# Optimization experiments

Measured on AMD Instinct MI355X. Metric: run time of the kernel, lower is better.

## Reference

```python
import jax, jax.numpy as jnp
import numpy as np

VOCAB, EMB, HDIM, VDIM, ATT = 30000, 256, 512, 128, 256
B, N, T = 64, 196, 32


def setup_inputs() -> dict:
    key = jax.random.key(0)
    ks = jax.random.split(key, 8)
    s = 0.02
    return {
        "V": jax.random.normal(ks[0], (B, N, VDIM), jnp.float32),
        "y": jax.random.randint(ks[1], (B, T), 0, VOCAB),
        "embed": jax.random.normal(ks[2], (VOCAB, EMB), jnp.float32) * s,
        "att_W_w": jax.random.normal(ks[3], (ATT, HDIM), jnp.float32) * s,
        "att_W_b": jnp.zeros((ATT,), jnp.float32),
        "att_U_w": jax.random.normal(ks[4], (ATT, VDIM), jnp.float32) * s,
        "att_U_b": jnp.zeros((ATT,), jnp.float32),
        "att_v_w": jax.random.normal(ks[5], (1, ATT), jnp.float32) * s,
        "att_v_b": jnp.zeros((1,), jnp.float32),
        "W_ih": jax.random.normal(ks[6], (4 * HDIM, EMB + VDIM), jnp.float32) * s,
        "W_hh": jax.random.normal(ks[7], (4 * HDIM, HDIM), jnp.float32) * s,
        "b_ih": jnp.zeros((4 * HDIM,), jnp.float32),
        "b_hh": jnp.zeros((4 * HDIM,), jnp.float32),
        "proj_w": jax.random.normal(jax.random.fold_in(key, 9), (EMB, HDIM), jnp.float32) * s,
    }


def reference(V, y, embed, att_W_w, att_W_b, att_U_w, att_U_b, att_v_w, att_v_b,
              W_ih, W_hh, b_ih, b_hh, proj_w):
    Bsz = y.shape[0]
    hdim = W_hh.shape[1]
    # loop-invariant U(V): [B, N, ATT]
    UV = jnp.einsum('bnv,av->bna', V, att_U_w) + att_U_b

    def step(carry, y_t):
        h, c, x_t = carry
        # additive attention
        Wh = h @ att_W_w.T + att_W_b                      # [B, ATT]
        e = jnp.tanh(Wh[:, None, :] + UV) @ att_v_w.T + att_v_b  # [B, N, 1]
        a = jax.nn.softmax(e, axis=1)
        ctx = jnp.sum(a * V, axis=1)                      # [B, VDIM]
        # LSTMCell (PyTorch gate order i, f, g, o)
        xc = jnp.concatenate([x_t, ctx], axis=-1)
        gates = xc @ W_ih.T + b_ih + h @ W_hh.T + b_hh
        i, f, g, o = jnp.split(gates, 4, axis=-1)
        c_new = jax.nn.sigmoid(f) * c + jax.nn.sigmoid(i) * jnp.tanh(g)
        h_new = jax.nn.sigmoid(o) * jnp.tanh(c_new)
        # dropout is identity in eval mode
        e_t = h_new @ proj_w.T                            # [B, EMB]
        logit = e_t @ embed.T                             # [B, VOCAB]
        x_next = embed[y_t]                               # teacher forcing
        return (h_new, c_new, x_next), logit

    h0 = jnp.zeros((Bsz, hdim), V.dtype)
    c0 = jnp.zeros((Bsz, hdim), V.dtype)
    x0 = embed[y[:, 0]]
    _, logits = jax.lax.scan(step, (h0, c0, x0), y[:, 1:].T)  # [T-1, B, VOCAB]
    return jnp.transpose(logits, (1, 0, 2))
```

## Files before the change

### kernel.cpp

```cpp
#include <hip/hip_runtime.h>
#include <stdint.h>

typedef unsigned short u16;
typedef uint32_t u32;
typedef short s16x8 __attribute__((ext_vector_type(8)));
typedef float f32x4 __attribute__((ext_vector_type(4)));

#define DEV __device__ __forceinline__

#define TSCALE 2.885390082f

DEV float bf2f(u16 h){ union{u32 u; float f;} x; x.u = ((u32)h)<<16; return x.f; }
DEV u16 f2bf(float f){ union{float f; u32 u;} x; x.f = f; u32 u = x.u;
  return (u16)((u + 0x7fffu + ((u>>16)&1u))>>16); }
DEV float bflo(u32 w){ union{u32 u; float f;} x; x.u = w<<16; return x.f; }
DEV float bfhi(u32 w){ union{u32 u; float f;} x; x.u = w & 0xffff0000u; return x.f; }

DEV float exp2_fast(float x){ return __builtin_amdgcn_exp2f(x); }
DEV float rcp_fast(float x){ return __builtin_amdgcn_rcpf(x); }
DEV float tanh2(float x){ float t = exp2_fast(TSCALE*x);
  return fmaf(-2.f, rcp_fast(t + 1.f), 1.f); }
DEV float sig2(float x){ return rcp_fast(1.f + exp2_fast(-1.442695041f*x)); }

DEV u32   ld_u(const u32* p){ return __hip_atomic_load(p, __ATOMIC_RELAXED, __HIP_MEMORY_SCOPE_AGENT); }
DEV void  st_u(u32* p, u32 v){ __hip_atomic_store(p, v, __ATOMIC_RELAXED, __HIP_MEMORY_SCOPE_AGENT); }

__global__ void f2b_kernel(const float* __restrict__ src, u16* __restrict__ dst, int n4, float scale){
  int i = blockIdx.x*blockDim.x + threadIdx.x;
  if (i < n4) {
    float4 v = ((const float4*)src)[i];
    ushort4 o; o.x = f2bf(v.x*scale); o.y = f2bf(v.y*scale); o.z = f2bf(v.z*scale); o.w = f2bf(v.w*scale);
    ((ushort4*)dst)[i] = o;
  }
}

__global__ void prep_wih2b(const float* __restrict__ Wih, u16* __restrict__ Wc){
  int idx = blockIdx.x*256 + threadIdx.x;
  int j = idx>>7, k = idx&127;
  Wc[idx] = f2bf(Wih[(size_t)j*384 + 256 + k]);
}

__global__ void repack_h(const u16* __restrict__ H2, u16* __restrict__ Hl){
  int r = blockIdx.x;
  int s = r>>6, b = r&63;
  int tid = threadIdx.x;
  u32 v = *((const u32*)(H2 + (size_t)(s+1)*32768 + (size_t)(tid>>2)*512 + (size_t)b*8) + (tid&3));
  ((u32*)(Hl + (size_t)r*512))[tid] = v;
}

__global__ __launch_bounds__(256) void gemm_bt(
    const u16* __restrict__ A, int lda,
    const u16* __restrict__ B, int ldb,
    const float* __restrict__ bias1, const float* __restrict__ bias2, float bscale,
    void* __restrict__ C, int ldc,
    int M, int N, int K, int Mt, int mode)
{
  __shared__ __align__(16) u16 As[64*64];
  __shared__ __align__(16) u16 Bs[128*64];
  int nwg = (int)gridDim.x;
  int b0 = blockIdx.x;
  int qq = nwg >> 3, rr = nwg & 7;
  int bswz;
  if (qq == 0) bswz = b0;
  else {
    int xcd = b0 & 7, i = b0 >> 3;
    bswz = (xcd < rr) ? (xcd*(qq+1) + i) : (rr*(qq+1) + (xcd - rr)*qq + i);
  }
  int mt = bswz % Mt, nt = bswz / Mt;
  int m0 = mt*64, n0 = nt*128;
  int tid = threadIdx.x, wave = tid>>6, lane = tid&63;
  int lrow = lane>>3, lcol = (lane&7)*8;
  f32x4 acc[2][4];
  #pragma unroll
  for (int i=0;i<2;i++)
    #pragma unroll
    for (int j=0;j<4;j++) acc[i][j] = (f32x4){0,0,0,0};
  int wm = (wave>>1)*32, wn = (wave&1)*64;
  int fr = lane&15, fk = (lane>>4)*8;
  for (int k0 = 0; k0 < K; k0 += 64) {
    __syncthreads();
    #pragma unroll
    for (int i = 0; i < 2; i++) {
      int ci = wave + i*4;
      int row = ci*8 + lrow;
      const u16* g = A + (size_t)(m0+row)*lda + k0 + lcol;
      __builtin_amdgcn_global_load_lds(
        (const __attribute__((address_space(1))) u32*)g,
        (__attribute__((address_space(3))) u32*)&As[ci*512], 16, 0, 0);
    }
    #pragma unroll
    for (int i = 0; i < 4; i++) {
      int ci = wave + i*4;
      int row = ci*8 + lrow;
      int gr = n0 + row; gr = gr < N ? gr : N-1;
      const u16* g = B + (size_t)gr*ldb + k0 + lcol;
      __builtin_amdgcn_global_load_lds(
        (const __attribute__((address_space(1))) u32*)g,
        (__attribute__((address_space(3))) u32*)&Bs[ci*512], 16, 0, 0);
    }
    __syncthreads();
    #pragma unroll
    for (int kk = 0; kk < 2; kk++) {
      s16x8 af[2], bfv[4];
      #pragma unroll
      for (int mi=0; mi<2; mi++)
        af[mi] = *(const s16x8*)&As[(wm + mi*16 + fr)*64 + kk*32 + fk];
      #pragma unroll
      for (int ni=0; ni<4; ni++)
        bfv[ni] = *(const s16x8*)&Bs[(wn + ni*16 + fr)*64 + kk*32 + fk];
      #pragma unroll
      for (int mi=0; mi<2; mi++)
        #pragma unroll
        for (int ni=0; ni<4; ni++)
          acc[mi][ni] = __builtin_amdgcn_mfma_f32_16x16x32_bf16(af[mi], bfv[ni], acc[mi][ni], 0,0,0);
    }
  }
  #pragma unroll
  for (int mi=0; mi<2; mi++)
    #pragma unroll
    for (int ni=0; ni<4; ni++) {
      int col = n0 + wn + ni*16 + (lane&15);
      if (col >= N) continue;
      float bv = 0.0f;
      if (bias1) bv += bias1[col];
      if (bias2) bv += bias2[col];
      bv *= bscale;
      int rbase = m0 + wm + mi*16 + ((lane>>4)<<2);
      #pragma unroll
      for (int r=0; r<4; r++) {
        int row = rbase + r;
        float v = acc[mi][ni][r] + bv;
        if (mode == 0) ((float*)C)[(size_t)row*ldc + col] = v;
        else if (mode == 1) ((u16*)C)[(size_t)row*ldc + col] = f2bf(v);
        else { int orow = (row&63)*31 + (row>>6); ((float*)C)[(size_t)orow*ldc + col] = v; }
      }
    }
}

__global__ void gather_x(const int* __restrict__ y, const float* __restrict__ embed, u16* __restrict__ X)
{
  int r = blockIdx.x;
  int s = r>>6, b = r&63;
  int tok = y[b*32 + s];
  X[(size_t)r*256 + threadIdx.x] = f2bf(embed[(size_t)tok*256 + threadIdx.x]);
}

#define NB 64

DEV void gbar(u32* flags, int bid, unsigned g){
  __asm__ volatile("" ::: "memory");
  __builtin_amdgcn_s_waitcnt(0);
  __syncthreads();
  if (threadIdx.x == 0) st_u(&flags[bid*16], g);
  if (threadIdx.x < 64) {
    for (;;) {
      u32 a = ld_u(&flags[threadIdx.x*16]);
      if (__all(a >= g)) break;
      __builtin_amdgcn_s_sleep(1);
    }
  }
  __syncthreads();
  __asm__ volatile("" ::: "memory");
}

__global__ __launch_bounds__(256, 1) void decoder_steps(
    const float* __restrict__ V,
    const float* __restrict__ attWb,
    const float* __restrict__ attvw,
    const float* __restrict__ attvb,
    const u16* __restrict__ WhhB,
    const u16* __restrict__ attWwB,
    const u16* __restrict__ WcB,
    u16* __restrict__ H2,
    const u16* __restrict__ UV,
    const u16* __restrict__ Xg,
    u16* __restrict__ CtxB,
    u32* __restrict__ flags)
{
  int bid = blockIdx.x, tid = threadIdx.x;
  int wave = tid>>6, lane = tid&63;
  int fr = lane&15, fkq = lane>>4;

  __shared__ __align__(16) u16 Wlds[32][648];
  __shared__ __align__(16) u16 Xglds[64][32];
  __shared__ float hls[512];
  __shared__ float whs[256];
  __shared__ float vws[256];
  __shared__ float esc[200];
  __shared__ float red1;
  __shared__ float part[256];

  {
    int r = tid>>3, p = tid&7;
    int grow = ((r>>3)<<9) + bid*8 + (r&7);
    #pragma unroll
    for (int i=0;i<10;i++){
      int k = p*80 + i*8;
      const u16* src = (k < 512) ? (WhhB + (size_t)grow*512 + k)
                                 : (WcB  + (size_t)grow*128 + (k-512));
      *(s16x8*)&Wlds[r][k] = *(const s16x8*)src;
    }
  }
  vws[tid] = attvw[tid];
  float vb = attvb[0];
  float c_reg[4] = {0.f,0.f,0.f,0.f};
  unsigned gen = 0;
  __syncthreads();

  int br = wave*16 + fr;

  for (int t = 0; t < 31; t++) {
    u32 hv = *((const u32*)(H2 + (size_t)t*32768 + (size_t)(tid>>2)*512 + (size_t)bid*8) + (tid&3));
    const u16* Hbase = H2 + (size_t)t*32768 + (size_t)br*8;
    s16x8 af[16];
    #pragma unroll
    for (int kt=0;kt<16;kt++) af[kt] = *(const s16x8*)(Hbase + (size_t)(kt*4+fkq)*512);
    s16x8 xg = *(const s16x8*)(Xg + (size_t)t*131072 + (size_t)(tid>>2)*2048 + (size_t)(tid&3)*512 + (size_t)bid*8);

    hls[2*tid]   = bflo(hv);
    hls[2*tid+1] = bfhi(hv);
    __syncthreads();

    {
      const u32* wr = (const u32*)(attWwB + (size_t)tid*512);
      float acc = TSCALE * attWb[tid];
      #pragma unroll 4
      for (int k=0;k<512;k+=8){
        u32 w0 = wr[(k>>1)+0], w1 = wr[(k>>1)+1], w2 = wr[(k>>1)+2], w3 = wr[(k>>1)+3];
        float4 h0 = *(const float4*)&hls[k];
        float4 h1 = *(const float4*)&hls[k+4];
        acc = fmaf(bflo(w0), h0.x, acc); acc = fmaf(bfhi(w0), h0.y, acc);
        acc = fmaf(bflo(w1), h0.z, acc); acc = fmaf(bfhi(w1), h0.w, acc);
        acc = fmaf(bflo(w2), h1.x, acc); acc = fmaf(bfhi(w2), h1.y, acc);
        acc = fmaf(bflo(w3), h1.z, acc); acc = fmaf(bfhi(w3), h1.w, acc);
      }
      whs[tid] = acc;
    }

    f32x4 a0 = (f32x4){0,0,0,0}, a1 = (f32x4){0,0,0,0};
    #pragma unroll
    for (int kt=0;kt<16;kt++){
      s16x8 b0 = *(const s16x8*)&Wlds[fr][kt*32 + fkq*8];
      s16x8 b1 = *(const s16x8*)&Wlds[16+fr][kt*32 + fkq*8];
      a0 = __builtin_amdgcn_mfma_f32_16x16x32_bf16(af[kt], b0, a0, 0,0,0);
      a1 = __builtin_amdgcn_mfma_f32_16x16x32_bf16(af[kt], b1, a1, 0,0,0);
    }
    __builtin_amdgcn_sched_barrier(0);
    __syncthreads();

    if (tid < 196) {
      const u32* uvp = (const u32*)(UV + ((size_t)bid*196 + tid)*256);
      float e = 0.0f;
      #pragma unroll 4
      for (int a = 0; a < 256; a += 4) {
        u32 uw0 = uvp[(a>>1)], uw1 = uvp[(a>>1)+1];
        float4 w4 = *(const float4*)&whs[a];
        float4 v4 = *(const float4*)&vws[a];
        float t0 = exp2_fast(w4.x + bflo(uw0));
        float t1 = exp2_fast(w4.y + bfhi(uw0));
        float t2 = exp2_fast(w4.z + bflo(uw1));
        float t3 = exp2_fast(w4.w + bfhi(uw1));
        e = fmaf(v4.x, fmaf(-2.f, rcp_fast(t0+1.f), 1.f), e);
        e = fmaf(v4.y, fmaf(-2.f, rcp_fast(t1+1.f), 1.f), e);
        e = fmaf(v4.z, fmaf(-2.f, rcp_fast(t2+1.f), 1.f), e);
        e = fmaf(v4.w, fmaf(-2.f, rcp_fast(t3+1.f), 1.f), e);
      }
      esc[tid] = exp2_fast(1.442695041f*(e + vb));
    }
    *(s16x8*)&Xglds[tid>>2][(tid&3)*8] = xg;
    __syncthreads();

    if (tid < 64) {
      float s = esc[tid] + esc[64+tid] + esc[128+tid];
      if (tid < 4)  s += esc[192+tid];
      #pragma unroll
      for (int off=32; off>=1; off>>=1) s += __shfl_xor(s, off);
      if (tid==0) red1 = s;
    }
    {
      int k = tid&127, hf = tid>>7;
      const float* vp = V + ((size_t)bid*196 + hf*98)*128 + k;
      float a = 0.f;
      for (int n2=0; n2<98; n2++) a = fmaf(esc[hf*98+n2], vp[(size_t)n2*128], a);
      part[tid] = a;
    }
    __syncthreads();

    if (tid < 64) {
      float inv = rcp_fast(red1);
      float c0 = (part[2*tid]   + part[128+2*tid]) * inv;
      float c1 = (part[2*tid+1] + part[129+2*tid]) * inv;
      u32 pk = (u32)f2bf(c0) | ((u32)f2bf(c1) << 16);
      st_u((u32*)(CtxB + (size_t)t*8192 + (size_t)bid*128) + tid, pk);
    }
    gen++; gbar(flags, bid, gen);

    {
      const u16* Crow = CtxB + (size_t)t*8192 + (size_t)br*128 + fkq*8;
      #pragma unroll
      for (int kt=0;kt<4;kt++){
        s16x8 cf = *(const s16x8*)(Crow + kt*32);
        s16x8 b0 = *(const s16x8*)&Wlds[fr][(16+kt)*32 + fkq*8];
        s16x8 b1 = *(const s16x8*)&Wlds[16+fr][(16+kt)*32 + fkq*8];
        a0 = __builtin_amdgcn_mfma_f32_16x16x32_bf16(cf, b0, a0, 0,0,0);
        a1 = __builtin_amdgcn_mfma_f32_16x16x32_bf16(cf, b1, a1, 0,0,0);
      }
      int c = fr;
      int xr0 = ((c>>3)&1)*8 + (c&7);
      float v0[4], v1[4], s0[4], s1[4];
      #pragma unroll
      for (int r=0;r<4;r++){
        int b_r = wave*16 + fkq*4 + r;
        v0[r] = a0[r] + bf2f(Xglds[b_r][xr0]);
        v1[r] = a1[r] + bf2f(Xglds[b_r][16+xr0]);
      }
      #pragma unroll
      for (int r=0;r<4;r++){ s0[r] = __shfl_xor(v0[r], 8); s1[r] = __shfl_xor(v1[r], 8); }
      if (c < 8) {
        #pragma unroll
        for (int r=0;r<4;r++){
          int b_r = wave*16 + fkq*4 + r;
          float ig = sig2(v0[r]);
          float fg = sig2(s0[r]);
          float gg = tanh2(v1[r]);
          float og = sig2(s1[r]);
          float cn = fmaf(fg, c_reg[r], ig*gg);
          c_reg[r] = cn;
          float hvv = og * tanh2(cn);
          float hp = __shfl_xor(hvv, 1);
          if (!(c&1)) {
            u32 pk = (u32)f2bf(hvv) | ((u32)f2bf(hp) << 16);
            st_u((u32*)(H2 + (size_t)(t+1)*32768 + (size_t)bid*512 + (size_t)b_r*8) + (c>>1), pk);
          }
        }
      }
    }
    if (t < 30) { gen++; gbar(flags, bid, gen); }
  }
}

#define OFF_H    1024u
#define OFF_UV   2098176u
#define OFF_X    8520704u
#define OFF_XG   9536512u
#define OFF_GH   17662976u
#define OFF_EMB  OFF_GH
#define OFF_WH   33915904u
#define OFF_E    35947520u
#define OFF_VB   36963328u
#define OFF_WIH  40174592u
#define OFF_WHH  41747456u
#define OFF_AWW  43844608u
#define OFF_AUW  44106752u
#define OFF_PRJ  44172288u

extern "C" void kernel_launch(void* const* d_in, const int* in_sizes, int n_in,
                              void* d_out, int out_size, void* d_ws, size_t ws_size,
                              hipStream_t stream)
{
  const float* V      = (const float*)d_in[0];
  const int*   y      = (const int*)  d_in[1];
  const float* embed  = (const float*)d_in[2];
  const float* attWw  = (const float*)d_in[3];
  const float* attWb  = (const float*)d_in[4];
  const float* attUw  = (const float*)d_in[5];
  const float* attUb  = (const float*)d_in[6];
  const float* attvw  = (const float*)d_in[7];
  const float* attvb  = (const float*)d_in[8];
  const float* Wih    = (const float*)d_in[9];
  const float* Whh    = (const float*)d_in[10];
  const float* bih    = (const float*)d_in[11];
  const float* bhh    = (const float*)d_in[12];
  const float* projw  = (const float*)d_in[13];
  float* out = (float*)d_out;
  char* ws = (char*)d_ws;

  u16*   H2   = (u16*)  (ws + OFF_H);
  u16*   UVb  = (u16*)  (ws + OFF_UV);
  u16*   Xb   = (u16*)  (ws + OFF_X);
  u16*   Xg   = (u16*)  (ws + OFF_XG);
  u16*   Hl   = (u16*)  (ws + OFF_XG);
  u32*   flags= (u32*)  (ws + OFF_WH);
  u16*   CtxB = (u16*)  (ws + OFF_WH + 8192);
  u16*   E    = (u16*)  (ws + OFF_E);
  u16*   Vb   = (u16*)  (ws + OFF_VB);
  u16*   WcB  = (u16*)  (ws + OFF_VB);
  u16*   embB = (u16*)  (ws + OFF_EMB);
  u16*   WihB = (u16*)  (ws + OFF_WIH);
  u16*   WhhB = (u16*)  (ws + OFF_WHH);
  u16*   attWwB = (u16*)(ws + OFF_AWW);
  u16*   attUwB = (u16*)(ws + OFF_AUW);
  u16*   projB  = (u16*)(ws + OFF_PRJ);

  hipMemsetAsync(ws + OFF_H, 0, 65536, stream);
  hipMemsetAsync(ws + OFF_WH, 0, 4096, stream);

  f2b_kernel<<<(401408+255)/256, 256, 0, stream>>>(V,     Vb,     401408, 1.0f);
  f2b_kernel<<<(196608+255)/256, 256, 0, stream>>>(Wih,   WihB,   196608, 1.0f);
  f2b_kernel<<<(262144+255)/256, 256, 0, stream>>>(Whh,   WhhB,   262144, 1.0f);
  f2b_kernel<<<(32768+255)/256,  256, 0, stream>>>(attWw, attWwB,  32768, TSCALE);
  f2b_kernel<<<(8192+255)/256,   256, 0, stream>>>(attUw, attUwB,   8192, TSCALE);
  f2b_kernel<<<(32768+255)/256,  256, 0, stream>>>(projw, projB,   32768, 1.0f);

  gather_x<<<1984, 256, 0, stream>>>(y, embed, Xb);

  gemm_bt<<<196*2, 256, 0, stream>>>(Vb, 128, attUwB, 128, attUb, nullptr, TSCALE,
                                     UVb, 256, 12544, 256, 128, 196, 1);
  prep_wih2b<<<1024, 256, 0, stream>>>(Wih, WcB);
  gemm_bt<<<31*16, 256, 0, stream>>>(Xb, 256, WihB, 384, bih, bhh, 1.0f,
                                     Xg, 2048, 1984, 2048, 256, 31, 1);

  decoder_steps<<<NB, 256, 0, stream>>>(V, attWb, attvw, attvb,
      WhhB, attWwB, WcB, H2, UVb, Xg, CtxB, flags);

  f2b_kernel<<<(1920000+255)/256, 256, 0, stream>>>(embed, embB, 1920000, 1.0f);

  repack_h<<<1984, 256, 0, stream>>>(H2, Hl);

  gemm_bt<<<31*2, 256, 0, stream>>>(Hl, 512, projB, 512, nullptr, nullptr, 1.0f,
                                    E, 256, 1984, 256, 512, 31, 1);
  gemm_bt<<<31*235, 256, 0, stream>>>(E, 256, embB, 256, nullptr, nullptr, 1.0f,
                                      out, 30000, 1984, 30000, 256, 31, 2);
}
```

Before: 1.015 ms.

## Double decoder block width to 512 threads and split attention reductions

The persistent decoder kernel now runs 512 threads per block instead of 256. The extra waves take over the H/Xg staging loads while the first four waves load MFMA fragments. The W·h matvec and the attention energy loop are each split in half across thread pairs and combined with a shuffle, and the context reduction is split four ways over the N dimension. This is meant to shorten the serial per-step latency on the 64-block critical path, at the cost of more threads idling during the MFMA phases and extra barrier participants. The embedding bf16 conversion is also moved to run before the decoder instead of after it, which only reorders independent work.

```diff
diff --git a/kernel.cpp b/kernel.cpp
--- a/kernel.cpp
+++ b/kernel.cpp
@@ -163,7 +163,7 @@
   __asm__ volatile("" ::: "memory");
 }
 
-__global__ __launch_bounds__(256, 1) void decoder_steps(
+__global__ __launch_bounds__(512, 1) void decoder_steps(
     const float* __restrict__ V,
     const float* __restrict__ attWb,
     const float* __restrict__ attvw,
@@ -188,20 +188,20 @@
   __shared__ float vws[256];
   __shared__ float esc[200];
   __shared__ float red1;
-  __shared__ float part[256];
+  __shared__ float part[512];
 
   {
-    int r = tid>>3, p = tid&7;
+    int r = tid>>4, p = tid&15;
     int grow = ((r>>3)<<9) + bid*8 + (r&7);
     #pragma unroll
-    for (int i=0;i<10;i++){
-      int k = p*80 + i*8;
+    for (int i=0;i<5;i++){
+      int k = p*40 + i*8;
       const u16* src = (k < 512) ? (WhhB + (size_t)grow*512 + k)
                                  : (WcB  + (size_t)grow*128 + (k-512));
       *(s16x8*)&Wlds[r][k] = *(const s16x8*)src;
     }
   }
-  vws[tid] = attvw[tid];
+  if (tid < 256) vws[tid] = attvw[tid];
   float vb = attvb[0];
   float c_reg[4] = {0.f,0.f,0.f,0.f};
   unsigned gen = 0;
@@ -210,64 +210,78 @@
   int br = wave*16 + fr;
 
   for (int t = 0; t < 31; t++) {
-    u32 hv = *((const u32*)(H2 + (size_t)t*32768 + (size_t)(tid>>2)*512 + (size_t)bid*8) + (tid&3));
-    const u16* Hbase = H2 + (size_t)t*32768 + (size_t)br*8;
     s16x8 af[16];
-    #pragma unroll
-    for (int kt=0;kt<16;kt++) af[kt] = *(const s16x8*)(Hbase + (size_t)(kt*4+fkq)*512);
-    s16x8 xg = *(const s16x8*)(Xg + (size_t)t*131072 + (size_t)(tid>>2)*2048 + (size_t)(tid&3)*512 + (size_t)bid*8);
-
-    hls[2*tid]   = bflo(hv);
-    hls[2*tid+1] = bfhi(hv);
+    s16x8 xg;
+    if (tid < 256) {
+      const u16* Hbase = H2 + (size_t)t*32768 + (size_t)br*8;
+      #pragma unroll
+      for (int kt=0;kt<16;kt++) af[kt] = *(const s16x8*)(Hbase + (size_t)(kt*4+fkq)*512);
+    } else {
+      int t2 = tid - 256;
+      u32 hv = *((const u32*)(H2 + (size_t)t*32768 + (size_t)(t2>>2)*512 + (size_t)bid*8) + (t2&3));
+      hls[2*t2]   = bflo(hv);
+      hls[2*t2+1] = bfhi(hv);
+      xg = *(const s16x8*)(Xg + (size_t)t*131072 + (size_t)(t2>>2)*2048 + (size_t)(t2&3)*512 + (size_t)bid*8);
+    }
     __syncthreads();
 
     {
-      const u32* wr = (const u32*)(attWwB + (size_t)tid*512);
-      float acc = TSCALE * attWb[tid];
+      int a_ = tid>>1, kh = (tid&1)*256;
+      const u32* wr = (const u32*)(attWwB + (size_t)a_*512 + kh);
+      float acc = (tid&1) ? 0.f : TSCALE * attWb[a_];
       #pragma unroll 4
-      for (int k=0;k<512;k+=8){
+      for (int k=0;k<256;k+=8){
         u32 w0 = wr[(k>>1)+0], w1 = wr[(k>>1)+1], w2 = wr[(k>>1)+2], w3 = wr[(k>>1)+3];
-        float4 h0 = *(const float4*)&hls[k];
-        float4 h1 = *(const float4*)&hls[k+4];
+        float4 h0 = *(const float4*)&hls[kh+k];
+        float4 h1 = *(const float4*)&hls[kh+k+4];
         acc = fmaf(bflo(w0), h0.x, acc); acc = fmaf(bfhi(w0), h0.y, acc);
         acc = fmaf(bflo(w1), h0.z, acc); acc = fmaf(bfhi(w1), h0.w, acc);
         acc = fmaf(bflo(w2), h1.x, acc); acc = fmaf(bfhi(w2), h1.y, acc);
         acc = fmaf(bflo(w3), h1.z, acc); acc = fmaf(bfhi(w3), h1.w, acc);
       }
-      whs[tid] = acc;
+      acc += __shfl_xor(acc, 1);
+      if (!(tid&1)) whs[a_] = acc;
     }
 
     f32x4 a0 = (f32x4){0,0,0,0}, a1 = (f32x4){0,0,0,0};
-    #pragma unroll
-    for (int kt=0;kt<16;kt++){
-      s16x8 b0 = *(const s16x8*)&Wlds[fr][kt*32 + fkq*8];
-      s16x8 b1 = *(const s16x8*)&Wlds[16+fr][kt*32 + fkq*8];
-      a0 = __builtin_amdgcn_mfma_f32_16x16x32_bf16(af[kt], b0, a0, 0,0,0);
-      a1 = __builtin_amdgcn_mfma_f32_16x16x32_bf16(af[kt], b1, a1, 0,0,0);
-    }
-    __builtin_amdgcn_sched_barrier(0);
-    __syncthreads();
-
-    if (tid < 196) {
-      const u32* uvp = (const u32*)(UV + ((size_t)bid*196 + tid)*256);
-      float e = 0.0f;
+    if (tid < 256) {
+      #pragma unroll
+      for (int kt=0;kt<16;kt++){
+        s16x8 b0 = *(const s16x8*)&Wlds[fr][kt*32 + fkq*8];
+        s16x8 b1 = *(const s16x8*)&Wlds[16+fr][kt*32 + fkq*8];
+        a0 = __builtin_amdgcn_mfma_f32_16x16x32_bf16(af[kt], b0, a0, 0,0,0);
+        a1 = __builtin_amdgcn_mfma_f32_16x16x32_bf16(af[kt], b1, a1, 0,0,0);
+      }
+      __builtin_amdgcn_sched_barrier(0);
+    }
+    __syncthreads();
+
+    if (tid < 392) {
+      int n = tid>>1, kh = (tid&1)*128;
+      const u32* uvp = (const u32*)(UV + ((size_t)bid*196 + n)*256 + kh);
+      float e0 = 0.0f, e1 = 0.0f;
       #pragma unroll 4
-      for (int a = 0; a < 256; a += 4) {
+      for (int a = 0; a < 128; a += 4) {
         u32 uw0 = uvp[(a>>1)], uw1 = uvp[(a>>1)+1];
-        float4 w4 = *(const float4*)&whs[a];
-        float4 v4 = *(const float4*)&vws[a];
+        float4 w4 = *(const float4*)&whs[kh+a];
+        float4 v4 = *(const float4*)&vws[kh+a];
         float t0 = exp2_fast(w4.x + bflo(uw0));
         float t1 = exp2_fast(w4.y + bfhi(uw0));
         float t2 = exp2_fast(w4.z + bflo(uw1));
         float t3 = exp2_fast(w4.w + bfhi(uw1));
-        e = fmaf(v4.x, fmaf(-2.f, rcp_fast(t0+1.f), 1.f), e);
-        e = fmaf(v4.y, fmaf(-2.f, rcp_fast(t1+1.f), 1.f), e);
-        e = fmaf(v4.z, fmaf(-2.f, rcp_fast(t2+1.f), 1.f), e);
-        e = fmaf(v4.w, fmaf(-2.f, rcp_fast(t3+1.f), 1.f), e);
-      }
-      esc[tid] = exp2_fast(1.442695041f*(e + vb));
-    }
-    *(s16x8*)&Xglds[tid>>2][(tid&3)*8] = xg;
+        e0 = fmaf(v4.x, fmaf(-2.f, rcp_fast(t0+1.f), 1.f), e0);
+        e1 = fmaf(v4.y, fmaf(-2.f, rcp_fast(t1+1.f), 1.f), e1);
+        e0 = fmaf(v4.z, fmaf(-2.f, rcp_fast(t2+1.f), 1.f), e0);
+        e1 = fmaf(v4.w, fmaf(-2.f, rcp_fast(t3+1.f), 1.f), e1);
+      }
+      float e = e0 + e1;
+      e += __shfl_xor(e, 1);
+      if (!(tid&1)) esc[n] = exp2_fast(1.442695041f*(e + vb));
+    }
+    if (tid >= 256) {
+      int t2 = tid - 256;
+      *(s16x8*)&Xglds[t2>>2][(t2&3)*8] = xg;
+    }
     __syncthreads();
 
     if (tid < 64) {
@@ -278,24 +292,24 @@
       if (tid==0) red1 = s;
     }
     {
-      int k = tid&127, hf = tid>>7;
-      const float* vp = V + ((size_t)bid*196 + hf*98)*128 + k;
+      int k = tid&127, q4 = tid>>7;
+      const float* vp = V + ((size_t)bid*196 + q4*49)*128 + k;
       float a = 0.f;
-      for (int n2=0; n2<98; n2++) a = fmaf(esc[hf*98+n2], vp[(size_t)n2*128], a);
+      for (int n2=0; n2<49; n2++) a = fmaf(esc[q4*49+n2], vp[(size_t)n2*128], a);
       part[tid] = a;
     }
     __syncthreads();
 
     if (tid < 64) {
       float inv = rcp_fast(red1);
-      float c0 = (part[2*tid]   + part[128+2*tid]) * inv;
-      float c1 = (part[2*tid+1] + part[129+2*tid]) * inv;
+      float c0 = (part[2*tid]   + part[128+2*tid] + part[256+2*tid] + part[384+2*tid]) * inv;
+      float c1 = (part[2*tid+1] + part[129+2*tid] + part[257+2*tid] + part[385+2*tid]) * inv;
       u32 pk = (u32)f2bf(c0) | ((u32)f2bf(c1) << 16);
       st_u((u32*)(CtxB + (size_t)t*8192 + (size_t)bid*128) + tid, pk);
     }
     gen++; gbar(flags, bid, gen);
 
-    {
+    if (tid < 256) {
       const u16* Crow = CtxB + (size_t)t*8192 + (size_t)br*128 + fkq*8;
       #pragma unroll
       for (int kt=0;kt<4;kt++){
@@ -401,6 +415,7 @@
   f2b_kernel<<<(32768+255)/256,  256, 0, stream>>>(attWw, attWwB,  32768, TSCALE);
   f2b_kernel<<<(8192+255)/256,   256, 0, stream>>>(attUw, attUwB,   8192, TSCALE);
   f2b_kernel<<<(32768+255)/256,  256, 0, stream>>>(projw, projB,   32768, 1.0f);
+  f2b_kernel<<<(1920000+255)/256, 256, 0, stream>>>(embed, embB, 1920000, 1.0f);
 
   gather_x<<<1984, 256, 0, stream>>>(y, embed, Xb);
 
@@ -410,10 +425,8 @@
   gemm_bt<<<31*16, 256, 0, stream>>>(Xb, 256, WihB, 384, bih, bhh, 1.0f,
                                      Xg, 2048, 1984, 2048, 256, 31, 1);
 
-  decoder_steps<<<NB, 256, 0, stream>>>(V, attWb, attvw, attvb,
+  decoder_steps<<<NB, 512, 0, stream>>>(V, attWb, attvw, attvb,
       WhhB, attWwB, WcB, H2, UVb, Xg, CtxB, flags);
-
-  f2b_kernel<<<(1920000+255)/256, 256, 0, stream>>>(embed, embB, 1920000, 1.0f);
 
   repack_h<<<1984, 256, 0, stream>>>(H2, Hl);
 
```

Measured after the change: 968.5 us. 4.6% less time.
